# Kernel tuning notes

Hardware: AMD Instinct MI355X
Metric: run time of the kernel (lower is better)

Reference implementation:

```python
import jax, jax.numpy as jnp
import numpy as np

ND, NT = 30000, 15000
FD, FT = 200, 570
H = 768
E_DD, E_DT, E_TT = 300000, 400000, 200000
NEG_SLOPE = 0.2


def _gat(x_src, x_dst, src, dst, Ws, Wd, a_s, a_d, b, n_dst):
    # PyG GATConv, heads=1: hs = lin_src(x_src), hd = lin_dst(x_dst)
    hs = x_src @ Ws                       # [Ns, H]
    hd = x_dst @ Wd                       # [Nd, H]
    es = hs @ a_s                         # [Ns]
    ed = hd @ a_d                         # [Nd]
    e = jax.nn.leaky_relu(es[src] + ed[dst], negative_slope=NEG_SLOPE)  # [E]
    m = jax.ops.segment_max(e, dst, num_segments=n_dst)
    m = jnp.where(jnp.isfinite(m), m, 0.0)
    w = jnp.exp(e - m[dst])
    s = jax.ops.segment_sum(w, dst, num_segments=n_dst)
    alpha = w / (s[dst] + 1e-16)
    out = jax.ops.segment_sum(hs[src] * alpha[:, None], dst, num_segments=n_dst)  # [n_dst, H]
    return out + b


def _layer(xd, xt, dd_src, dd_dst, dt_src, dt_dst, tt_src, tt_dst, p):
    nd, nt = xd.shape[0], xt.shape[0]
    sl_d = jnp.arange(nd, dtype=dd_src.dtype)
    sl_t = jnp.arange(nt, dtype=tt_src.dtype)
    # add_self_loops=True for the homogeneous relations d-d and t-t
    dds = jnp.concatenate([dd_src, sl_d]); ddd = jnp.concatenate([dd_dst, sl_d])
    tts = jnp.concatenate([tt_src, sl_t]); ttd = jnp.concatenate([tt_dst, sl_t])
    o_dd = _gat(xd, xd, dds, ddd, p['Wsrc_dd'], p['Wdst_dd'], p['asrc_dd'], p['adst_dd'], p['b_dd'], nd)
    o_rv = _gat(xt, xd, dt_dst, dt_src, p['Wsrc_rv'], p['Wdst_rv'], p['asrc_rv'], p['adst_rv'], p['b_rv'], nd)
    o_dt = _gat(xd, xt, dt_src, dt_dst, p['Wsrc_dt'], p['Wdst_dt'], p['asrc_dt'], p['adst_dt'], p['b_dt'], nt)
    o_tt = _gat(xt, xt, tts, ttd, p['Wsrc_tt'], p['Wdst_tt'], p['asrc_tt'], p['adst_tt'], p['b_tt'], nt)
    # HeteroConv aggr='sum', then relu per node type
    return jax.nn.relu(o_dd + o_rv), jax.nn.relu(o_dt + o_tt)


def setup_inputs() -> dict:
    key = jax.random.key(0)
    ks = jax.random.split(key, 40)
    d = {}
    d['drug_x'] = jax.random.normal(ks[0], (ND, FD), jnp.float32)
    d['target_x'] = jax.random.normal(ks[1], (NT, FT), jnp.float32)
    d['dd_src'] = jax.random.randint(ks[2], (E_DD,), 0, ND, jnp.int32)
    d['dd_dst'] = jax.random.randint(ks[3], (E_DD,), 0, ND, jnp.int32)
    d['dt_src'] = jax.random.randint(ks[4], (E_DT,), 0, ND, jnp.int32)
    d['dt_dst'] = jax.random.randint(ks[5], (E_DT,), 0, NT, jnp.int32)
    d['tt_src'] = jax.random.randint(ks[6], (E_TT,), 0, NT, jnp.int32)
    d['tt_dst'] = jax.random.randint(ks[7], (E_TT,), 0, NT, jnp.int32)
    d['drug_mask'] = jax.random.randint(ks[8], (ND, 1), 0, 2, jnp.int32)
    d['target_mask'] = jax.random.randint(ks[9], (NT, 1), 0, 2, jnp.int32)
    d['mask_drug'] = 0.05 * jax.random.normal(ks[10], (1, FD), jnp.float32)
    d['mask_target'] = 0.05 * jax.random.normal(ks[11], (1, FT), jnp.float32)
    i = 12
    for rel, fin_s, fin_d in [('dd', FD, FD), ('dt', FD, FT), ('rv', FT, FD), ('tt', FT, FT)]:
        d['Wsrc_' + rel] = 0.05 * jax.random.normal(ks[i], (fin_s, H), jnp.float32); i += 1
        d['Wdst_' + rel] = 0.05 * jax.random.normal(ks[i], (fin_d, H), jnp.float32); i += 1
        d['asrc_' + rel] = 0.05 * jax.random.normal(ks[i], (H,), jnp.float32); i += 1
        d['adst_' + rel] = 0.05 * jax.random.normal(ks[i], (H,), jnp.float32); i += 1
        d['b_' + rel] = jnp.zeros((H,), jnp.float32)
    return d


def reference(drug_x, target_x, dd_src, dd_dst, dt_src, dt_dst, tt_src, tt_dst,
              drug_mask, target_mask, mask_drug, mask_target,
              Wsrc_dd, Wdst_dd, asrc_dd, adst_dd, b_dd,
              Wsrc_dt, Wdst_dt, asrc_dt, adst_dt, b_dt,
              Wsrc_rv, Wdst_rv, asrc_rv, adst_rv, b_rv,
              Wsrc_tt, Wdst_tt, asrc_tt, adst_tt, b_tt):
    p = dict(Wsrc_dd=Wsrc_dd, Wdst_dd=Wdst_dd, asrc_dd=asrc_dd, adst_dd=adst_dd, b_dd=b_dd,
             Wsrc_dt=Wsrc_dt, Wdst_dt=Wdst_dt, asrc_dt=asrc_dt, adst_dt=adst_dt, b_dt=b_dt,
             Wsrc_rv=Wsrc_rv, Wdst_rv=Wdst_rv, asrc_rv=asrc_rv, adst_rv=adst_rv, b_rv=b_rv,
             Wsrc_tt=Wsrc_tt, Wdst_tt=Wdst_tt, asrc_tt=asrc_tt, adst_tt=adst_tt, b_tt=b_tt)
    xd, xt = _layer(drug_x, target_x, dd_src, dd_dst, dt_src, dt_dst, tt_src, tt_dst, p)
    # MAE branch: replace masked node features with learned mask token, rerun conv
    dm = drug_mask.astype(jnp.float32)
    tm = target_mask.astype(jnp.float32)
    _dx = drug_x * (1.0 - dm) + dm * mask_drug
    _tx = target_x * (1.0 - tm) + tm * mask_target
    _xd, _xt = _layer(_dx, _tx, dd_src, dd_dst, dt_src, dt_dst, tt_src, tt_dst, p)
    loss_mae = (((xd - _xd) ** 2) * dm).sum() / (dm.sum() * H + 1e-16) \
             + (((xt - _xt) ** 2) * tm).sum() / (tm.sum() * H + 1e-16)
    return (xd, xt, loss_mae)
```

## Files before the change

### kernel.cpp

```cpp
#include <hip/hip_runtime.h>
#include <hip/hip_bf16.h>

#define ND 30000
#define NT 15000
#define FD 200
#define FT 570
#define HDIM 768
#define EDD 300000
#define EDT 400000
#define ETT 200000

#define KPD 256
#define KPT 576
#define KPA 832

#define BM 128
#define BN 128
#define GBK 64
#define MTD ((ND + BM - 1) / BM)
#define MTT ((NT + BM - 1) / BM)

typedef __attribute__((ext_vector_type(8))) short short8;
typedef __attribute__((ext_vector_type(4))) float float4v;


__device__ __forceinline__ float ldx(const void* p, size_t i, int f32) {
  return f32 ? ((const float*)p)[i]
             : __bfloat162float(((const __hip_bfloat16*)p)[i]);
}
__device__ __forceinline__ void stx(void* p, size_t i, int f32, float v) {
  if (f32) ((float*)p)[i] = v;
  else     ((__hip_bfloat16*)p)[i] = __float2bfloat16(v);
}
__device__ __forceinline__ float b2f(unsigned short u) {
  return __uint_as_float(((unsigned)u) << 16);
}
__device__ __forceinline__ unsigned short f2b(float f) {
  __hip_bfloat16 h = __float2bfloat16(f);
  return *(unsigned short*)&h;
}
__device__ __forceinline__ unsigned pk2(float a, float b) {
  return (unsigned)f2b(a) | ((unsigned)f2b(b) << 16);
}

__device__ __forceinline__ float wave_reduce(float v) {
#pragma unroll
  for (int off = 32; off > 0; off >>= 1) v += __shfl_xor(v, off, 64);
  return v;
}

__global__ void sniff(const void* x, int* flag) {
  int t = threadIdx.x;
  float cnt = 0.f;
  for (int i = t; i < 8192; i += 256) {
    float v = __bfloat162float(((const __hip_bfloat16*)x)[i]);
    if (!(fabsf(v) < 100.f)) cnt += 1.f;
  }
  cnt = wave_reduce(cnt);
  __shared__ float red[4];
  if ((t & 63) == 0) red[t >> 6] = cnt;
  __syncthreads();
  if (t == 0) flag[0] = (red[0] + red[1] + red[2] + red[3] > 256.f) ? 1 : 0;
}

__global__ __launch_bounds__(256) void wa_dot8(
    const void* W0, const void* W1, const void* W2, const void* W3,
    const void* W4, const void* W5, const void* W6, const void* W7,
    const void* a0, const void* a1, const void* a2, const void* a3,
    const void* a4, const void* a5, const void* a6, const void* a7,
    float* __restrict__ vaD, float* __restrict__ vaT,
    const int* __restrict__ flag) {
  const void* Ws[8] = {W0, W1, W2, W3, W4, W5, W6, W7};
  const void* as[8] = {a0, a1, a2, a3, a4, a5, a6, a7};
  int f32 = flag[0];
  int wid = (blockIdx.x * 256 + threadIdx.x) >> 6;
  int lane = threadIdx.x & 63;
  const void* W; const void* a; float* out; int k;
  if (wid < 4 * FD) {
    int q = wid / FD; k = wid - q * FD;
    W = Ws[q]; a = as[q]; out = vaD + q * FD + k;
  } else {
    int w2 = wid - 4 * FD;
    if (w2 >= 4 * FT) return;
    int q = w2 / FT; k = w2 - q * FT;
    W = Ws[4 + q]; a = as[4 + q]; out = vaT + q * FT + k;
  }
  float acc = 0.f;
  for (int h = lane; h < HDIM; h += 64)
    acc += ldx(W, (size_t)k * HDIM + h, f32) * ldx(a, h, f32);
  acc = wave_reduce(acc);
  if (lane == 0) *out = acc;
}

__global__ void tok_dots(const void* __restrict__ tok1, const void* __restrict__ tok2,
                         const float* __restrict__ vaD, const float* __restrict__ vaT,
                         float* __restrict__ ts, const int* __restrict__ flag) {
  int w = threadIdx.x >> 6;
  int lane = threadIdx.x & 63;
  int f32 = flag[0];
  float acc = 0.f;
  if (w < 4) {
    for (int k = lane; k < FD; k += 64) acc += ldx(tok1, k, f32) * vaD[w * FD + k];
  } else {
    int q = w - 4;
    for (int k = lane; k < FT; k += 64) acc += ldx(tok2, k, f32) * vaT[q * FT + k];
  }
  acc = wave_reduce(acc);
  if (lane == 0) {
    const int map[8] = {0, 1, 3, 4, 2, 5, 6, 7};
    ts[map[w]] = acc;
  }
}

__global__ __launch_bounds__(256) void row_dot4(const void* __restrict__ x,
                                                const float* __restrict__ va,
                                                float* __restrict__ outv, int N, int K,
                                                const int* __restrict__ flag) {
  int f32 = flag[0];
  int row = (blockIdx.x * 256 + threadIdx.x) >> 6;
  int lane = threadIdx.x & 63;
  if (row >= N) return;
  float a0 = 0.f, a1 = 0.f, a2 = 0.f, a3 = 0.f;
  for (int k = lane; k < K; k += 64) {
    float v = ldx(x, (size_t)row * K + k, f32);
    a0 += v * va[k];
    a1 += v * va[K + k];
    a2 += v * va[2 * K + k];
    a3 += v * va[3 * K + k];
  }
  a0 = wave_reduce(a0); a1 = wave_reduce(a1);
  a2 = wave_reduce(a2); a3 = wave_reduce(a3);
  if (lane == 0) {
    float* o = outv + (size_t)row * 4;
    o[0] = a0; o[1] = a1; o[2] = a2; o[3] = a3;
  }
}

__global__ __launch_bounds__(256) void pack_a(const void* __restrict__ x,
                                              unsigned short* __restrict__ Aout,
                                              int M, int K, int Kp,
                                              const int* __restrict__ flag) {
  int f32 = flag[0];
  long long gid = (long long)blockIdx.x * 256 + threadIdx.x;
  long long total = (long long)M * Kp / 4;
  if (gid >= total) return;
  long long e0 = gid * 4;
  int row = (int)(e0 / Kp);
  int k = (int)(e0 % Kp);
  ushort4 o;
  unsigned short r[4];
#pragma unroll
  for (int c = 0; c < 4; ++c) {
    int kk = k + c;
    float f = 0.f;
    if (kk < K) f = ldx(x, (size_t)row * K + kk, f32);
    r[c] = f2b(f);
  }
  o.x = r[0]; o.y = r[1]; o.z = r[2]; o.w = r[3];
  *(ushort4*)(Aout + e0) = o;
}

__global__ __launch_bounds__(256) void pack_bTa(const void* __restrict__ W1,
                                                const void* __restrict__ W2,
                                                unsigned short* __restrict__ Bout,
                                                const int* __restrict__ flag) {
  int f32 = flag[0];
  long long gid = (long long)blockIdx.x * 256 + threadIdx.x;
  long long total = (long long)HDIM * KPA / 4;
  if (gid >= total) return;
  long long e0 = gid * 4;
  int n = (int)(e0 / KPA);
  int k = (int)(e0 % KPA);
  ushort4 o;
  unsigned short r[4];
#pragma unroll
  for (int c = 0; c < 4; ++c) {
    int kk = k + c;
    float f = 0.f;
    if (kk < 256) {
      if (kk < FD) f = ldx(W1, (size_t)kk * HDIM + n, f32);
    } else {
      int k2 = kk - 256;
      if (k2 < FT) f = ldx(W2, (size_t)k2 * HDIM + n, f32);
    }
    r[c] = f2b(f);
  }
  o.x = r[0]; o.y = r[1]; o.z = r[2]; o.w = r[3];
  *(ushort4*)(Bout + e0) = o;
}

__global__ void zero_i32(int* __restrict__ p, int n) {
  int i = blockIdx.x * 256 + threadIdx.x;
  if (i < n) p[i] = 0;
}

__global__ void count4(const int* __restrict__ dd_dst, const int* __restrict__ dt_src,
                       const int* __restrict__ dt_dst, const int* __restrict__ tt_dst,
                       int* __restrict__ c_dd, int* __restrict__ c_rv,
                       int* __restrict__ c_dt, int* __restrict__ c_tt) {
  int i = blockIdx.x * 256 + threadIdx.x;
  if (i < EDD + ND) { int d = (i < EDD) ? dd_dst[i] : i - EDD; atomicAdd(&c_dd[d], 1); return; }
  i -= EDD + ND;
  if (i < EDT) { atomicAdd(&c_rv[dt_src[i]], 1); return; }
  i -= EDT;
  if (i < EDT) { atomicAdd(&c_dt[dt_dst[i]], 1); return; }
  i -= EDT;
  if (i < ETT + NT) { int d = (i < ETT) ? tt_dst[i] : i - ETT; atomicAdd(&c_tt[d], 1); }
}

__global__ __launch_bounds__(256) void scan6(
    const int* __restrict__ a0, int n0, int* __restrict__ o0,
    const int* __restrict__ a1, int n1, int* __restrict__ o1,
    const int* __restrict__ a2, int n2, int* __restrict__ o2,
    const int* __restrict__ a3, int n3, int* __restrict__ o3,
    const int* __restrict__ a4, int n4, int* __restrict__ o4,
    const int* __restrict__ a5, int n5, int* __restrict__ o5) {
  const int* a; int n; int* o;
  switch (blockIdx.x) {
    case 0: a = a0; n = n0; o = o0; break;
    case 1: a = a1; n = n1; o = o1; break;
    case 2: a = a2; n = n2; o = o2; break;
    case 3: a = a3; n = n3; o = o3; break;
    case 4: a = a4; n = n4; o = o4; break;
    default: a = a5; n = n5; o = o5; break;
  }
  __shared__ int part[256];
  int t = threadIdx.x;
  int strip = (n + 255) / 256;
  int lo = min(t * strip, n), hi = min(lo + strip, n);
  int s = 0;
  for (int i = lo; i < hi; ++i) s += a[i];
  part[t] = s;
  __syncthreads();
  if (t == 0) {
    int run = 0;
    for (int i = 0; i < 256; ++i) { int v = part[i]; part[i] = run; run += v; }
  }
  __syncthreads();
  int run = part[t];
  for (int i = lo; i < hi; ++i) { o[i] = run; run += a[i]; }
  if (hi == n) o[n] = run;
}

__global__ void ridx2(const int* __restrict__ mD, const int* __restrict__ cD,
                      int* __restrict__ rD,
                      const int* __restrict__ mT, const int* __restrict__ cT,
                      int* __restrict__ rT) {
  int i = blockIdx.x * 256 + threadIdx.x;
  if (i < ND) { if (mD[i] != 0) rD[cD[i]] = i; return; }
  i -= ND;
  if (i < NT) { if (mT[i] != 0) rT[cT[i]] = i; }
}

__global__ void fill4(const int* __restrict__ dd_src, const int* __restrict__ dd_dst,
                      const int* __restrict__ dt_src, const int* __restrict__ dt_dst,
                      const int* __restrict__ tt_src, const int* __restrict__ tt_dst,
                      const int* __restrict__ rp_dd, int* __restrict__ f_dd, int* __restrict__ ei_dd,
                      const int* __restrict__ rp_rv, int* __restrict__ f_rv, int* __restrict__ ei_rv,
                      const int* __restrict__ rp_dt, int* __restrict__ f_dt, int* __restrict__ ei_dt,
                      const int* __restrict__ rp_tt, int* __restrict__ f_tt, int* __restrict__ ei_tt) {
  int i = blockIdx.x * 256 + threadIdx.x;
  if (i < EDD + ND) {
    int s, d;
    if (i < EDD) { s = dd_src[i]; d = dd_dst[i]; } else { s = d = i - EDD; }
    ei_dd[rp_dd[d] + atomicAdd(&f_dd[d], 1)] = s;
    return;
  }
  i -= EDD + ND;
  if (i < EDT) {
    int d = dt_src[i], s = dt_dst[i];
    ei_rv[rp_rv[d] + atomicAdd(&f_rv[d], 1)] = s;
    return;
  }
  i -= EDT;
  if (i < EDT) {
    int d = dt_dst[i], s = dt_src[i];
    ei_dt[rp_dt[d] + atomicAdd(&f_dt[d], 1)] = s;
    return;
  }
  i -= EDT;
  if (i < ETT + NT) {
    int s, d;
    if (i < ETT) { s = tt_src[i]; d = tt_dst[i]; } else { s = d = i - ETT; }
    ei_tt[rp_tt[d] + atomicAdd(&f_tt[d], 1)] = s;
  }
}


__device__ __forceinline__ void fma4(float* acc, uint2 A, float al) {
  unsigned w;
  w = A.x; acc[0] += al * __uint_as_float(w << 16); acc[1] += al * __uint_as_float(w & 0xffff0000u);
  w = A.y; acc[2] += al * __uint_as_float(w << 16); acc[3] += al * __uint_as_float(w & 0xffff0000u);
}

__device__ __forceinline__ float lrexp(float v) {
  v = (v >= 0.f) ? v : 0.2f * v;
  return __expf(v);
}

__global__ __launch_bounds__(256) void gat_agg2(
    const int* __restrict__ rp1, const int* __restrict__ ei1,
    const unsigned short* __restrict__ A1, const int* __restrict__ msk1,
    const void* __restrict__ tok1,
    const float* __restrict__ es1, const float* __restrict__ ed1,
    const int* __restrict__ rp2, const int* __restrict__ ei2,
    const unsigned short* __restrict__ A2, const int* __restrict__ msk2,
    const void* __restrict__ tok2,
    const float* __restrict__ es2, const float* __restrict__ ed2,
    const float* __restrict__ ts,
    int N, const int* __restrict__ mdst, const int* __restrict__ cidx,
    unsigned short* __restrict__ agg1, unsigned short* __restrict__ agg2,
    const int* __restrict__ flag) {
  int wid = (blockIdx.x * 256 + threadIdx.x) >> 6;
  int lane = threadIdx.x & 63;
  if (wid >= N) return;
  int f32 = flag[0];
  bool need2 = (mdst[wid] != 0);
  float ac1[13], ac2[13];
#pragma unroll
  for (int c = 0; c < 13; ++c) { ac1[c] = 0.f; ac2[c] = 0.f; }

  {
    float tes = ts[0], ted = ts[1];
    int lo = rp1[wid], hi = rp1[wid + 1];
    float edA = ed1[4 * (size_t)wid];
    float s1 = 0.f, s2 = 0.f;
    for (int e = lo + lane; e < hi; e += 64) {
      int sn = ei1[e];
      float ev = es1[4 * (size_t)sn];
      s1 += lrexp(ev + edA);
      if (need2) {
        float e2 = (msk1[sn] != 0) ? tes : ev;
        s2 += lrexp(e2 + ted);
      }
    }
    s1 = wave_reduce(s1);
    float i1 = 1.f / (s1 + 1e-16f), i2 = 0.f;
    if (need2) { s2 = wave_reduce(s2); i2 = 1.f / (s2 + 1e-16f); }
    float wt = 0.f;
    int pn = (lo < hi) ? ei1[lo] : 0;
    for (int e = lo; e < hi; ++e) {
      int sn = __builtin_amdgcn_readfirstlane(pn);
      if (e + 1 < hi) pn = ei1[e + 1];
      uint2 rv = *(const uint2*)(A1 + (size_t)sn * KPD + 4 * lane);
      float ev = es1[4 * (size_t)sn];
      fma4(ac1, rv, lrexp(ev + edA) * i1);
      if (need2) {
        if (msk1[sn] != 0) wt += lrexp(tes + ted) * i2;
        else fma4(ac2, rv, lrexp(ev + ted) * i2);
      }
    }
    if (need2) {
#pragma unroll
      for (int c = 0; c < 4; ++c) {
        int col = 4 * lane + c;
        float tv = (col < FD) ? ldx(tok1, col, f32) : 0.f;
        ac2[c] += wt * tv;
      }
    }
  }

  {
    float tes = ts[2], ted = ts[3];
    int lo = rp2[wid], hi = rp2[wid + 1];
    float edA = ed2[4 * (size_t)wid];
    float s1 = 0.f, s2 = 0.f;
    for (int e = lo + lane; e < hi; e += 64) {
      int sn = ei2[e];
      float ev = es2[4 * (size_t)sn];
      s1 += lrexp(ev + edA);
      if (need2) {
        float e2 = (msk2[sn] != 0) ? tes : ev;
        s2 += lrexp(e2 + ted);
      }
    }
    s1 = wave_reduce(s1);
    float i1 = 1.f / (s1 + 1e-16f), i2 = 0.f;
    if (need2) { s2 = wave_reduce(s2); i2 = 1.f / (s2 + 1e-16f); }
    float wt = 0.f;
    int pn = (lo < hi) ? ei2[lo] : 0;
    for (int e = lo; e < hi; ++e) {
      int sn = __builtin_amdgcn_readfirstlane(pn);
      if (e + 1 < hi) pn = ei2[e + 1];
      const unsigned short* row = A2 + (size_t)sn * KPT;
      uint2 ra = *(const uint2*)(row + 4 * lane);
      uint2 rb = *(const uint2*)(row + 256 + 4 * lane);
      unsigned short rc = row[512 + lane];
      float ev = es2[4 * (size_t)sn];
      float a1 = lrexp(ev + edA) * i1;
      fma4(ac1 + 4, ra, a1);
      fma4(ac1 + 8, rb, a1);
      ac1[12] += a1 * b2f(rc);
      if (need2) {
        if (msk2[sn] != 0) {
          wt += lrexp(tes + ted) * i2;
        } else {
          float a2 = lrexp(ev + ted) * i2;
          fma4(ac2 + 4, ra, a2);
          fma4(ac2 + 8, rb, a2);
          ac2[12] += a2 * b2f(rc);
        }
      }
    }
    if (need2) {
#pragma unroll
      for (int c = 0; c < 4; ++c) {
        int colA = 4 * lane + c;
        int colB = 256 + 4 * lane + c;
        ac2[4 + c] += wt * ldx(tok2, colA, f32);
        ac2[8 + c] += wt * ldx(tok2, colB, f32);
      }
      int colC = 512 + lane;
      ac2[12] += wt * ((colC < FT) ? ldx(tok2, colC, f32) : 0.f);
    }
  }

  unsigned short* o1 = agg1 + (size_t)wid * KPA;
  uint2 u;
  u.x = pk2(ac1[0], ac1[1]);  u.y = pk2(ac1[2], ac1[3]);  *(uint2*)(o1 + 4 * lane) = u;
  u.x = pk2(ac1[4], ac1[5]);  u.y = pk2(ac1[6], ac1[7]);  *(uint2*)(o1 + 256 + 4 * lane) = u;
  u.x = pk2(ac1[8], ac1[9]);  u.y = pk2(ac1[10], ac1[11]); *(uint2*)(o1 + 512 + 4 * lane) = u;
  o1[768 + lane] = f2b(ac1[12]);
  if (need2) {
    unsigned short* o2 = agg2 + (size_t)cidx[wid] * KPA;
    u.x = pk2(ac2[0], ac2[1]);  u.y = pk2(ac2[2], ac2[3]);  *(uint2*)(o2 + 4 * lane) = u;
    u.x = pk2(ac2[4], ac2[5]);  u.y = pk2(ac2[6], ac2[7]);  *(uint2*)(o2 + 256 + 4 * lane) = u;
    u.x = pk2(ac2[8], ac2[9]);  u.y = pk2(ac2[10], ac2[11]); *(uint2*)(o2 + 512 + 4 * lane) = u;
    o2[768 + lane] = f2b(ac2[12]);
  }
}


__global__ __launch_bounds__(256) void gemm2(
    const unsigned short* __restrict__ A0, const unsigned short* __restrict__ B0,
    const void* __restrict__ c1_0, const void* __restrict__ c2_0,
    int M0s, const int* __restrict__ mc0, const int* __restrict__ rx0,
    unsigned long long base0, float* __restrict__ pp0,
    const unsigned short* __restrict__ A1, const unsigned short* __restrict__ B1,
    const void* __restrict__ c1_1, const void* __restrict__ c2_1,
    int M1s, const int* __restrict__ mc1, const int* __restrict__ rx1,
    unsigned long long base1, float* __restrict__ pp1,
    int mt0, int nwg, void* __restrict__ out, int mode,
    const int* __restrict__ flag) {
  __shared__ unsigned long long lds8[8192];
  unsigned short* ldsS = (unsigned short*)lds8;
  float* Cls = (float*)lds8;

  int b = blockIdx.x;
  int q = nwg >> 3, r = nwg & 7;
  int xcd = b & 7, pos = b >> 3;
  int wg = (xcd < r ? xcd * (q + 1) : r * (q + 1) + (xcd - r) * q) + pos;
  int prob = (wg >= 6 * mt0) ? 1 : 0;
  int rel = prob ? (wg - 6 * mt0) : wg;
  int mt = rel / 6, nt = rel - mt * 6;

  const unsigned short* A = prob ? A1 : A0;
  const unsigned short* Bt = prob ? B1 : B0;
  const void* c1 = prob ? c1_1 : c1_0;
  const void* c2 = prob ? c2_1 : c2_0;
  const int* mc = prob ? mc1 : mc0;
  const int* ridx = prob ? rx1 : rx0;
  size_t base = prob ? base1 : base0;
  float* parts = prob ? pp1 : pp0;
  int M = prob ? M1s : M0s;
  if (mc) M = *mc;
  int m0 = mt * BM;
  if (m0 >= M) return;
  int n0 = nt * BN;

  int t = threadIdx.x;
  int wave = t >> 6, lane = t & 63;
  int quad = lane >> 4, l15 = lane & 15;
  int wrow = (wave & 1) * 64, wcol = (wave >> 1) * 64;
  float4v acc[4][4];
#pragma unroll
  for (int i = 0; i < 4; ++i)
#pragma unroll
    for (int j = 0; j < 4; ++j) acc[i][j] = (float4v){0.f, 0.f, 0.f, 0.f};

  auto stage = [&](int buf, int k0) {
#pragma unroll
    for (int i = 0; i < 4; ++i) {
      int chunk = (wave * 4 + i) * 64 + lane;
      int row = chunk >> 3;
      int cs = (chunk & 7) ^ (row & 7);
      const unsigned short* ga = A + (size_t)(m0 + row) * KPA + k0 + cs * 8;
      __builtin_amdgcn_global_load_lds(
          (const __attribute__((address_space(1))) unsigned int*)ga,
          (__attribute__((address_space(3))) unsigned int*)(ldsS + buf * 8192 + (wave * 4 + i) * 512),
          16, 0, 0);
      const unsigned short* gb = Bt + (size_t)(n0 + row) * KPA + k0 + cs * 8;
      __builtin_amdgcn_global_load_lds(
          (const __attribute__((address_space(1))) unsigned int*)gb,
          (__attribute__((address_space(3))) unsigned int*)(ldsS + 16384 + buf * 8192 + (wave * 4 + i) * 512),
          16, 0, 0);
    }
  };
  auto compute = [&](int buf) {
#pragma unroll
    for (int kk = 0; kk < 2; ++kk) {
      int kc = kk * 4 + quad;
      short8 a[4], bfr[4];
#pragma unroll
      for (int i = 0; i < 4; ++i) {
        int rr = wrow + i * 16 + l15;
        a[i] = *(const short8*)(ldsS + buf * 8192 + rr * 64 + ((kc ^ (rr & 7)) << 3));
      }
#pragma unroll
      for (int j = 0; j < 4; ++j) {
        int rr = wcol + j * 16 + l15;
        bfr[j] = *(const short8*)(ldsS + 16384 + buf * 8192 + rr * 64 + ((kc ^ (rr & 7)) << 3));
      }
#pragma unroll
      for (int i = 0; i < 4; ++i)
#pragma unroll
        for (int j = 0; j < 4; ++j)
          acc[i][j] = __builtin_amdgcn_mfma_f32_16x16x32_bf16(a[i], bfr[j], acc[i][j], 0, 0, 0);
    }
  };

  stage(0, 0);
  __syncthreads();
  int cur = 0;
#pragma unroll 1
  for (int ks = 1; ks < KPA / GBK; ++ks) {
    stage(cur ^ 1, ks * GBK);
    compute(cur);
    __syncthreads();
    cur ^= 1;
  }
  compute(cur);

  int f32 = flag[0];
  float bias[4];
#pragma unroll
  for (int j = 0; j < 4; ++j) {
    int n = n0 + wcol + j * 16 + l15;
    bias[j] = ldx(c1, n, f32) + ldx(c2, n, f32);
  }
  __syncthreads();
#pragma unroll
  for (int i = 0; i < 4; ++i) {
#pragma unroll
    for (int j = 0; j < 4; ++j) {
      int col = wcol + j * 16 + l15;
#pragma unroll
      for (int rr = 0; rr < 4; ++rr) {
        int row = wrow + i * 16 + quad * 4 + rr;
        float v = acc[i][j][rr] + bias[j];
        Cls[row * 128 + col] = v > 0.f ? v : 0.f;
      }
    }
  }
  __syncthreads();
  float cpart = 0.f;
#pragma unroll
  for (int i = 0; i < 16; ++i) {
    int ch = t + i * 256;
    int row = ch >> 5, cc = ch & 31;
    int m = m0 + row;
    if (m >= M) continue;
    float v0 = Cls[row * 128 + cc * 4 + 0];
    float v1 = Cls[row * 128 + cc * 4 + 1];
    float v2 = Cls[row * 128 + cc * 4 + 2];
    float v3 = Cls[row * 128 + cc * 4 + 3];
    int n = n0 + cc * 4;
    if (mode == 1) {
      size_t idx = base + (size_t)m * HDIM + n;
      if (f32) {
        *(float4v*)((float*)out + idx) = (float4v){v0, v1, v2, v3};
      } else {
        uint2 u; u.x = pk2(v0, v1); u.y = pk2(v2, v3);
        *(uint2*)((unsigned short*)out + idx) = u;
      }
    } else {
      int orig = ridx[m];
      size_t idx = base + (size_t)orig * HDIM + n;
      float d0, d1, d2, d3;
      if (f32) {
        float4v w = *(const float4v*)((const float*)out + idx);
        d0 = w[0] - v0; d1 = w[1] - v1; d2 = w[2] - v2; d3 = w[3] - v3;
      } else {
        uint2 u = *(const uint2*)((const unsigned short*)out + idx);
        d0 = __uint_as_float(u.x << 16) - v0;
        d1 = __uint_as_float(u.x & 0xffff0000u) - v1;
        d2 = __uint_as_float(u.y << 16) - v2;
        d3 = __uint_as_float(u.y & 0xffff0000u) - v3;
      }
      cpart += d0 * d0 + d1 * d1 + d2 * d2 + d3 * d3;
    }
  }
  if (mode == 2) {
    cpart = wave_reduce(cpart);
    if (lane == 0) atomicAdd(&parts[(wg * 4 + wave) & 2047], cpart);
  }
}

__global__ __launch_bounds__(256) void loss_final(const float* __restrict__ parts,
                                                  const int* __restrict__ cd,
                                                  const int* __restrict__ ct,
                                                  void* __restrict__ out, size_t off,
                                                  const int* __restrict__ flag) {
  float a = 0.f, b = 0.f;
  for (int i = threadIdx.x; i < 2048; i += 256) { a += parts[i]; b += parts[2048 + i]; }
  a = wave_reduce(a);
  b = wave_reduce(b);
  __shared__ float ra[4], rb[4];
  if ((threadIdx.x & 63) == 0) { ra[threadIdx.x >> 6] = a; rb[threadIdx.x >> 6] = b; }
  __syncthreads();
  if (threadIdx.x == 0) {
    float sd = ra[0] + ra[1] + ra[2] + ra[3];
    float st = rb[0] + rb[1] + rb[2] + rb[3];
    float loss = sd / ((float)cd[0] * (float)HDIM + 1e-16f)
               + st / ((float)ct[0] * (float)HDIM + 1e-16f);
    stx(out, off, flag[0], loss);
  }
}


extern "C" void kernel_launch(void* const* d_in, const int* in_sizes, int n_in,
                              void* d_out, int out_size, void* d_ws, size_t ws_size,
                              hipStream_t stream) {
  const void* drug_x    = d_in[0];
  const void* target_x  = d_in[1];
  const int* dd_src = (const int*)d_in[2];
  const int* dd_dst = (const int*)d_in[3];
  const int* dt_src = (const int*)d_in[4];
  const int* dt_dst = (const int*)d_in[5];
  const int* tt_src = (const int*)d_in[6];
  const int* tt_dst = (const int*)d_in[7];
  const int* drug_mask   = (const int*)d_in[8];
  const int* target_mask = (const int*)d_in[9];
  const void* mask_drug   = d_in[10];
  const void* mask_target = d_in[11];
  const void* Wsrc_dd = d_in[12]; const void* Wdst_dd = d_in[13];
  const void* asrc_dd = d_in[14]; const void* adst_dd = d_in[15];
  const void* b_dd    = d_in[16];
  const void* Wsrc_dt = d_in[17]; const void* Wdst_dt = d_in[18];
  const void* asrc_dt = d_in[19]; const void* adst_dt = d_in[20];
  const void* b_dt    = d_in[21];
  const void* Wsrc_rv = d_in[22]; const void* Wdst_rv = d_in[23];
  const void* asrc_rv = d_in[24]; const void* adst_rv = d_in[25];
  const void* b_rv    = d_in[26];
  const void* Wsrc_tt = d_in[27]; const void* Wdst_tt = d_in[28];
  const void* asrc_tt = d_in[29]; const void* adst_tt = d_in[30];
  const void* b_tt    = d_in[31];

  char* p = (char*)d_ws;
  auto alloc = [&](size_t bytes) -> void* {
    void* r = (void*)p;
    p += (bytes + 255) & ~(size_t)255;
    return r;
  };
  const size_t PAD = (size_t)BM * KPA * 2;
  unsigned short* Ad    = (unsigned short*)alloc((size_t)ND * KPD * 2);
  unsigned short* At    = (unsigned short*)alloc((size_t)NT * KPT * 2);
  unsigned short* aggd1 = (unsigned short*)alloc((size_t)ND * KPA * 2 + PAD);
  unsigned short* aggd2 = (unsigned short*)alloc((size_t)ND * KPA * 2 + PAD);
  unsigned short* aggt1 = (unsigned short*)alloc((size_t)NT * KPA * 2 + PAD);
  unsigned short* aggt2 = (unsigned short*)alloc((size_t)NT * KPA * 2 + PAD);
  unsigned short* BdW   = (unsigned short*)alloc((size_t)HDIM * KPA * 2);
  unsigned short* BtW   = (unsigned short*)alloc((size_t)HDIM * KPA * 2);
  float* dvec1 = (float*)alloc((size_t)ND * 4 * 4);
  float* tvec1 = (float*)alloc((size_t)NT * 4 * 4);
  int* rp_dd = (int*)alloc((size_t)(ND + 1) * 4);
  int* rp_rv = (int*)alloc((size_t)(ND + 1) * 4);
  int* rp_dt = (int*)alloc((size_t)(NT + 1) * 4);
  int* rp_tt = (int*)alloc((size_t)(NT + 1) * 4);
  int* ei_dd = (int*)alloc((size_t)(EDD + ND) * 4);
  int* ei_rv = (int*)alloc((size_t)EDT * 4);
  int* ei_dt = (int*)alloc((size_t)EDT * 4);
  int* ei_tt = (int*)alloc((size_t)(ETT + NT) * 4);
  const int ZN = 4 * (ND + NT) + 4096;
  int* zblock = (int*)alloc((size_t)ZN * 4);
  int* cnt_dd = zblock;
  int* cnt_rv = cnt_dd + ND;
  int* cnt_dt = cnt_rv + ND;
  int* cnt_tt = cnt_dt + NT;
  int* f_dd   = cnt_tt + NT;
  int* f_rv   = f_dd + ND;
  int* f_dt   = f_rv + ND;
  int* f_tt   = f_dt + NT;
  float* parts = (float*)(f_tt + NT);
  int* cidxD = (int*)alloc((size_t)(ND + 1) * 4);
  int* cidxT = (int*)alloc((size_t)(NT + 1) * 4);
  int* ridxD = (int*)alloc((size_t)ND * 4);
  int* ridxT = (int*)alloc((size_t)NT * 4);
  float* vaD = (float*)alloc((size_t)4 * FD * 4);
  float* vaT = (float*)alloc((size_t)4 * FT * 4);
  float* tokscal = (float*)alloc(64);
  int*   flag  = (int*)alloc(256);

  sniff<<<1, 256, 0, stream>>>(drug_x, flag);
  zero_i32<<<(ZN + 255) / 256, 256, 0, stream>>>(zblock, ZN);

  {
    int waves = 4 * FD + 4 * FT;
    wa_dot8<<<(waves * 64 + 255) / 256, 256, 0, stream>>>(
        Wsrc_dd, Wdst_dd, Wdst_rv, Wsrc_dt, Wsrc_rv, Wdst_dt, Wsrc_tt, Wdst_tt,
        asrc_dd, adst_dd, adst_rv, asrc_dt, asrc_rv, adst_dt, asrc_tt, adst_tt,
        vaD, vaT, flag);
    tok_dots<<<1, 512, 0, stream>>>(mask_drug, mask_target, vaD, vaT, tokscal, flag);
  }

  {
    int g = (int)(((long long)HDIM * KPA / 4 + 255) / 256);
    pack_bTa<<<g, 256, 0, stream>>>(Wsrc_dd, Wsrc_rv, BdW, flag);
    pack_bTa<<<g, 256, 0, stream>>>(Wsrc_dt, Wsrc_tt, BtW, flag);
  }

  {
    int total = (EDD + ND) + EDT + EDT + (ETT + NT);
    count4<<<(total + 255) / 256, 256, 0, stream>>>(dd_dst, dt_src, dt_dst, tt_dst,
                                                    cnt_dd, cnt_rv, cnt_dt, cnt_tt);
    scan6<<<6, 256, 0, stream>>>(cnt_dd, ND, rp_dd, cnt_rv, ND, rp_rv,
                                 cnt_dt, NT, rp_dt, cnt_tt, NT, rp_tt,
                                 drug_mask, ND, cidxD, target_mask, NT, cidxT);
    ridx2<<<(ND + NT + 255) / 256, 256, 0, stream>>>(drug_mask, cidxD, ridxD,
                                                     target_mask, cidxT, ridxT);
    fill4<<<(total + 255) / 256, 256, 0, stream>>>(dd_src, dd_dst, dt_src, dt_dst,
                                                   tt_src, tt_dst,
                                                   rp_dd, f_dd, ei_dd, rp_rv, f_rv, ei_rv,
                                                   rp_dt, f_dt, ei_dt, rp_tt, f_tt, ei_tt);
  }

  {
    long long ta = (long long)ND * KPD / 4;
    pack_a<<<(int)((ta + 255) / 256), 256, 0, stream>>>(drug_x, Ad, ND, FD, KPD, flag);
    ta = (long long)NT * KPT / 4;
    pack_a<<<(int)((ta + 255) / 256), 256, 0, stream>>>(target_x, At, NT, FT, KPT, flag);
  }
  row_dot4<<<(ND + 3) / 4, 256, 0, stream>>>(drug_x, vaD, dvec1, ND, FD, flag);
  row_dot4<<<(NT + 3) / 4, 256, 0, stream>>>(target_x, vaT, tvec1, NT, FT, flag);

  gat_agg2<<<(ND + 3) / 4, 256, 0, stream>>>(
      rp_dd, ei_dd, Ad, drug_mask, mask_drug, dvec1 + 0, dvec1 + 1,
      rp_rv, ei_rv, At, target_mask, mask_target, tvec1 + 0, dvec1 + 2,
      tokscal, ND, drug_mask, cidxD, aggd1, aggd2, flag);
  gat_agg2<<<(NT + 3) / 4, 256, 0, stream>>>(
      rp_dt, ei_dt, Ad, drug_mask, mask_drug, dvec1 + 3, tvec1 + 1,
      rp_tt, ei_tt, At, target_mask, mask_target, tvec1 + 2, tvec1 + 3,
      tokscal + 4, NT, target_mask, cidxT, aggt1, aggt2, flag);

  size_t baseT = (size_t)ND * HDIM;
  size_t baseL = baseT + (size_t)NT * HDIM;

  const int NWG = 6 * (MTD + MTT);
  gemm2<<<NWG, 256, 0, stream>>>(
      aggd1, BdW, b_dd, b_rv, ND, nullptr, nullptr, 0ULL, parts,
      aggt1, BtW, b_dt, b_tt, NT, nullptr, nullptr, (unsigned long long)baseT, parts,
      MTD, NWG, d_out, 1, flag);
  gemm2<<<NWG, 256, 0, stream>>>(
      aggd2, BdW, b_dd, b_rv, ND, cidxD + ND, ridxD, 0ULL, parts,
      aggt2, BtW, b_dt, b_tt, NT, cidxT + NT, ridxT, (unsigned long long)baseT, parts + 2048,
      MTD, NWG, d_out, 2, flag);

  loss_final<<<1, 256, 0, stream>>>(parts, cidxD + ND, cidxT + NT, d_out, baseL, flag);
}
```

Baseline: 923.5 us.

## Fuse pack/rowdot and agg launches, halve GEMM K-tile and LDS footprint

Merges the bf16 packing of the node features with the per-row attention dot products into one kernel, so each input row is read once. It also merges the two pack_bTa launches and the two gat_agg2 launches into single launches. The GEMM K-tile drops from 64 to 32 with a matching swizzle, which halves shared memory, and the epilogue now writes C through LDS in two 64-column halves. The aim is fewer launches, less input traffic and higher GEMM occupancy, at the cost of more K iterations and barriers in the GEMM.

```diff
diff --git a/kernel.cpp b/kernel.cpp
--- a/kernel.cpp
+++ b/kernel.cpp
@@ -16,7 +16,8 @@
 
 #define BM 128
 #define BN 128
-#define GBK 64
+#define GBK 32
+#define KTILES (KPA / GBK)
 #define MTD ((ND + BM - 1) / BM)
 #define MTT ((NT + BM - 1) / BM)
 
@@ -112,21 +113,45 @@
   }
 }
 
-__global__ __launch_bounds__(256) void row_dot4(const void* __restrict__ x,
-                                                const float* __restrict__ va,
-                                                float* __restrict__ outv, int N, int K,
-                                                const int* __restrict__ flag) {
+__global__ __launch_bounds__(256) void pack_rowdot(
+    const void* __restrict__ xD, const void* __restrict__ xT,
+    const float* __restrict__ vaD, const float* __restrict__ vaT,
+    unsigned short* __restrict__ Ad, unsigned short* __restrict__ At,
+    float* __restrict__ dvec, float* __restrict__ tvec,
+    const int* __restrict__ flag) {
+  int wid = (blockIdx.x * 256 + threadIdx.x) >> 6;
+  int lane = threadIdx.x & 63;
   int f32 = flag[0];
-  int row = (blockIdx.x * 256 + threadIdx.x) >> 6;
-  int lane = threadIdx.x & 63;
-  if (row >= N) return;
+  const void* x; const float* va; unsigned short* Aout; float* outv; int K, Kp, row;
+  if (wid < ND) { x = xD; va = vaD; Aout = Ad; outv = dvec; K = FD; Kp = KPD; row = wid; }
+  else if (wid < ND + NT) { x = xT; va = vaT; Aout = At; outv = tvec; K = FT; Kp = KPT; row = wid - ND; }
+  else return;
   float a0 = 0.f, a1 = 0.f, a2 = 0.f, a3 = 0.f;
-  for (int k = lane; k < K; k += 64) {
-    float v = ldx(x, (size_t)row * K + k, f32);
-    a0 += v * va[k];
-    a1 += v * va[K + k];
-    a2 += v * va[2 * K + k];
-    a3 += v * va[3 * K + k];
+  for (int it = 0; it * 256 < Kp; ++it) {
+    int base = 4 * lane + it * 256;
+    if (base >= Kp) continue;
+    ushort4 o;
+    unsigned short r[4];
+    float fv[4];
+#pragma unroll
+    for (int c = 0; c < 4; ++c) {
+      int kk = base + c;
+      float f = (kk < K) ? ldx(x, (size_t)row * K + kk, f32) : 0.f;
+      fv[c] = f;
+      r[c] = f2b(f);
+    }
+    o.x = r[0]; o.y = r[1]; o.z = r[2]; o.w = r[3];
+    *(ushort4*)(Aout + (size_t)row * Kp + base) = o;
+#pragma unroll
+    for (int c = 0; c < 4; ++c) {
+      int kk = base + c;
+      if (kk < K) {
+        a0 += fv[c] * va[kk];
+        a1 += fv[c] * va[K + kk];
+        a2 += fv[c] * va[2 * K + kk];
+        a3 += fv[c] * va[3 * K + kk];
+      }
+    }
   }
   a0 = wave_reduce(a0); a1 = wave_reduce(a1);
   a2 = wave_reduce(a2); a3 = wave_reduce(a3);
@@ -136,38 +161,17 @@
   }
 }
 
-__global__ __launch_bounds__(256) void pack_a(const void* __restrict__ x,
-                                              unsigned short* __restrict__ Aout,
-                                              int M, int K, int Kp,
-                                              const int* __restrict__ flag) {
+__global__ __launch_bounds__(256) void pack_bTa2(
+    const void* __restrict__ W1a, const void* __restrict__ W2a, unsigned short* __restrict__ Ba,
+    const void* __restrict__ W1b, const void* __restrict__ W2b, unsigned short* __restrict__ Bb,
+    const int* __restrict__ flag) {
   int f32 = flag[0];
+  long long one = (long long)HDIM * KPA / 4;
   long long gid = (long long)blockIdx.x * 256 + threadIdx.x;
-  long long total = (long long)M * Kp / 4;
-  if (gid >= total) return;
-  long long e0 = gid * 4;
-  int row = (int)(e0 / Kp);
-  int k = (int)(e0 % Kp);
-  ushort4 o;
-  unsigned short r[4];
-#pragma unroll
-  for (int c = 0; c < 4; ++c) {
-    int kk = k + c;
-    float f = 0.f;
-    if (kk < K) f = ldx(x, (size_t)row * K + kk, f32);
-    r[c] = f2b(f);
-  }
-  o.x = r[0]; o.y = r[1]; o.z = r[2]; o.w = r[3];
-  *(ushort4*)(Aout + e0) = o;
-}
-
-__global__ __launch_bounds__(256) void pack_bTa(const void* __restrict__ W1,
-                                                const void* __restrict__ W2,
-                                                unsigned short* __restrict__ Bout,
-                                                const int* __restrict__ flag) {
-  int f32 = flag[0];
-  long long gid = (long long)blockIdx.x * 256 + threadIdx.x;
-  long long total = (long long)HDIM * KPA / 4;
-  if (gid >= total) return;
+  if (gid >= 2 * one) return;
+  const void* W1; const void* W2; unsigned short* Bout;
+  if (gid < one) { W1 = W1a; W2 = W2a; Bout = Ba; }
+  else { W1 = W1b; W2 = W2b; Bout = Bb; gid -= one; }
   long long e0 = gid * 4;
   int n = (int)(e0 / KPA);
   int k = (int)(e0 % KPA);
@@ -286,7 +290,6 @@
   }
 }
 
-
 __device__ __forceinline__ void fma4(float* acc, uint2 A, float al) {
   unsigned w;
   w = A.x; acc[0] += al * __uint_as_float(w << 16); acc[1] += al * __uint_as_float(w & 0xffff0000u);
@@ -299,22 +302,45 @@
 }
 
 __global__ __launch_bounds__(256) void gat_agg2(
-    const int* __restrict__ rp1, const int* __restrict__ ei1,
-    const unsigned short* __restrict__ A1, const int* __restrict__ msk1,
-    const void* __restrict__ tok1,
-    const float* __restrict__ es1, const float* __restrict__ ed1,
-    const int* __restrict__ rp2, const int* __restrict__ ei2,
-    const unsigned short* __restrict__ A2, const int* __restrict__ msk2,
-    const void* __restrict__ tok2,
-    const float* __restrict__ es2, const float* __restrict__ ed2,
-    const float* __restrict__ ts,
-    int N, const int* __restrict__ mdst, const int* __restrict__ cidx,
-    unsigned short* __restrict__ agg1, unsigned short* __restrict__ agg2,
+    const unsigned short* __restrict__ A1, const unsigned short* __restrict__ A2,
+    const int* __restrict__ msk1, const int* __restrict__ msk2,
+    const void* __restrict__ tok1, const void* __restrict__ tok2,
+    const float* __restrict__ tokscal,
+    const int* __restrict__ rpD1, const int* __restrict__ eiD1,
+    const float* __restrict__ esD1, const float* __restrict__ edD1,
+    const int* __restrict__ rpD2, const int* __restrict__ eiD2,
+    const float* __restrict__ esD2, const float* __restrict__ edD2,
+    const int* __restrict__ cidxD,
+    unsigned short* __restrict__ aggd1, unsigned short* __restrict__ aggd2,
+    const int* __restrict__ rpT1, const int* __restrict__ eiT1,
+    const float* __restrict__ esT1, const float* __restrict__ edT1,
+    const int* __restrict__ rpT2, const int* __restrict__ eiT2,
+    const float* __restrict__ esT2, const float* __restrict__ edT2,
+    const int* __restrict__ cidxT,
+    unsigned short* __restrict__ aggt1, unsigned short* __restrict__ aggt2,
     const int* __restrict__ flag) {
-  int wid = (blockIdx.x * 256 + threadIdx.x) >> 6;
+  int gwid = (blockIdx.x * 256 + threadIdx.x) >> 6;
   int lane = threadIdx.x & 63;
-  if (wid >= N) return;
+  if (gwid >= ND + NT) return;
   int f32 = flag[0];
+
+  const int *rp1, *ei1, *rp2, *ei2, *cidx;
+  const float *es1, *ed1, *es2, *ed2, *ts;
+  const int* mdst;
+  unsigned short *agg1, *agg2;
+  int wid;
+  if (gwid < ND) {
+    wid = gwid; mdst = msk1;
+    rp1 = rpD1; ei1 = eiD1; es1 = esD1; ed1 = edD1;
+    rp2 = rpD2; ei2 = eiD2; es2 = esD2; ed2 = edD2;
+    cidx = cidxD; agg1 = aggd1; agg2 = aggd2; ts = tokscal;
+  } else {
+    wid = gwid - ND; mdst = msk2;
+    rp1 = rpT1; ei1 = eiT1; es1 = esT1; ed1 = edT1;
+    rp2 = rpT2; ei2 = eiT2; es2 = esT2; ed2 = edT2;
+    cidx = cidxT; agg1 = aggt1; agg2 = aggt2; ts = tokscal + 4;
+  }
+
   bool need2 = (mdst[wid] != 0);
   float ac1[13], ac2[13];
 #pragma unroll
@@ -442,7 +468,7 @@
     unsigned long long base1, float* __restrict__ pp1,
     int mt0, int nwg, void* __restrict__ out, int mode,
     const int* __restrict__ flag) {
-  __shared__ unsigned long long lds8[8192];
+  __shared__ unsigned long long lds8[4096];
   unsigned short* ldsS = (unsigned short*)lds8;
   float* Cls = (float*)lds8;
 
@@ -480,50 +506,46 @@
 
   auto stage = [&](int buf, int k0) {
 #pragma unroll
-    for (int i = 0; i < 4; ++i) {
-      int chunk = (wave * 4 + i) * 64 + lane;
-      int row = chunk >> 3;
-      int cs = (chunk & 7) ^ (row & 7);
+    for (int i = 0; i < 2; ++i) {
+      int chunk = (wave * 2 + i) * 64 + lane;
+      int row = chunk >> 2;
+      int cs = (chunk & 3) ^ ((row >> 1) & 3);
       const unsigned short* ga = A + (size_t)(m0 + row) * KPA + k0 + cs * 8;
       __builtin_amdgcn_global_load_lds(
           (const __attribute__((address_space(1))) unsigned int*)ga,
-          (__attribute__((address_space(3))) unsigned int*)(ldsS + buf * 8192 + (wave * 4 + i) * 512),
+          (__attribute__((address_space(3))) unsigned int*)(ldsS + buf * 4096 + (wave * 2 + i) * 512),
           16, 0, 0);
       const unsigned short* gb = Bt + (size_t)(n0 + row) * KPA + k0 + cs * 8;
       __builtin_amdgcn_global_load_lds(
           (const __attribute__((address_space(1))) unsigned int*)gb,
-          (__attribute__((address_space(3))) unsigned int*)(ldsS + 16384 + buf * 8192 + (wave * 4 + i) * 512),
+          (__attribute__((address_space(3))) unsigned int*)(ldsS + 8192 + buf * 4096 + (wave * 2 + i) * 512),
           16, 0, 0);
     }
   };
   auto compute = [&](int buf) {
-#pragma unroll
-    for (int kk = 0; kk < 2; ++kk) {
-      int kc = kk * 4 + quad;
-      short8 a[4], bfr[4];
-#pragma unroll
-      for (int i = 0; i < 4; ++i) {
-        int rr = wrow + i * 16 + l15;
-        a[i] = *(const short8*)(ldsS + buf * 8192 + rr * 64 + ((kc ^ (rr & 7)) << 3));
-      }
-#pragma unroll
-      for (int j = 0; j < 4; ++j) {
-        int rr = wcol + j * 16 + l15;
-        bfr[j] = *(const short8*)(ldsS + 16384 + buf * 8192 + rr * 64 + ((kc ^ (rr & 7)) << 3));
-      }
-#pragma unroll
-      for (int i = 0; i < 4; ++i)
-#pragma unroll
-        for (int j = 0; j < 4; ++j)
-          acc[i][j] = __builtin_amdgcn_mfma_f32_16x16x32_bf16(a[i], bfr[j], acc[i][j], 0, 0, 0);
-    }
+    short8 a[4], bfr[4];
+#pragma unroll
+    for (int i = 0; i < 4; ++i) {
+      int rr = wrow + i * 16 + l15;
+      a[i] = *(const short8*)(ldsS + buf * 4096 + rr * 32 + ((quad ^ ((rr >> 1) & 3)) << 3));
+    }
+#pragma unroll
+    for (int j = 0; j < 4; ++j) {
+      int rc = wcol + j * 16 + l15;
+      bfr[j] = *(const short8*)(ldsS + 8192 + buf * 4096 + rc * 32 + ((quad ^ ((rc >> 1) & 3)) << 3));
+    }
+#pragma unroll
+    for (int i = 0; i < 4; ++i)
+#pragma unroll
+      for (int j = 0; j < 4; ++j)
+        acc[i][j] = __builtin_amdgcn_mfma_f32_16x16x32_bf16(a[i], bfr[j], acc[i][j], 0, 0, 0);
   };
 
   stage(0, 0);
   __syncthreads();
   int cur = 0;
 #pragma unroll 1
-  for (int ks = 1; ks < KPA / GBK; ++ks) {
+  for (int ks = 1; ks < KTILES; ++ks) {
     stage(cur ^ 1, ks * GBK);
     compute(cur);
     __syncthreads();
@@ -538,56 +560,57 @@
     int n = n0 + wcol + j * 16 + l15;
     bias[j] = ldx(c1, n, f32) + ldx(c2, n, f32);
   }
-  __syncthreads();
-#pragma unroll
-  for (int i = 0; i < 4; ++i) {
-#pragma unroll
-    for (int j = 0; j < 4; ++j) {
-      int col = wcol + j * 16 + l15;
-#pragma unroll
-      for (int rr = 0; rr < 4; ++rr) {
-        int row = wrow + i * 16 + quad * 4 + rr;
-        float v = acc[i][j][rr] + bias[j];
-        Cls[row * 128 + col] = v > 0.f ? v : 0.f;
+  float cpart = 0.f;
+#pragma unroll
+  for (int h = 0; h < 2; ++h) {
+    __syncthreads();
+    if ((wave >> 1) == h) {
+#pragma unroll
+      for (int i = 0; i < 4; ++i)
+#pragma unroll
+        for (int j = 0; j < 4; ++j)
+#pragma unroll
+          for (int rr = 0; rr < 4; ++rr) {
+            int row = wrow + i * 16 + quad * 4 + rr;
+            int col = (j * 16 + l15) ^ (((row >> 2) & 1) << 4);
+            float v = acc[i][j][rr] + bias[j];
+            Cls[row * 64 + col] = v > 0.f ? v : 0.f;
+          }
+    }
+    __syncthreads();
+#pragma unroll
+    for (int i = 0; i < 8; ++i) {
+      int ch = t + i * 256;
+      int row = ch >> 4, cc = ch & 15;
+      int m = m0 + row;
+      if (m >= M) continue;
+      int scc = cc ^ (((row >> 2) & 1) << 2);
+      float4v v = *(const float4v*)(Cls + row * 64 + scc * 4);
+      int n = n0 + h * 64 + cc * 4;
+      if (mode == 1) {
+        size_t idx = base + (size_t)m * HDIM + n;
+        if (f32) {
+          *(float4v*)((float*)out + idx) = v;
+        } else {
+          uint2 u; u.x = pk2(v[0], v[1]); u.y = pk2(v[2], v[3]);
+          *(uint2*)((unsigned short*)out + idx) = u;
+        }
+      } else {
+        int orig = ridx[m];
+        size_t idx = base + (size_t)orig * HDIM + n;
+        float d0, d1, d2, d3;
+        if (f32) {
+          float4v w = *(const float4v*)((const float*)out + idx);
+          d0 = w[0] - v[0]; d1 = w[1] - v[1]; d2 = w[2] - v[2]; d3 = w[3] - v[3];
+        } else {
+          uint2 u = *(const uint2*)((const unsigned short*)out + idx);
+          d0 = __uint_as_float(u.x << 16) - v[0];
+          d1 = __uint_as_float(u.x & 0xffff0000u) - v[1];
+          d2 = __uint_as_float(u.y << 16) - v[2];
+          d3 = __uint_as_float(u.y & 0xffff0000u) - v[3];
+        }
+        cpart += d0 * d0 + d1 * d1 + d2 * d2 + d3 * d3;
       }
-    }
-  }
-  __syncthreads();
-  float cpart = 0.f;
-#pragma unroll
-  for (int i = 0; i < 16; ++i) {
-    int ch = t + i * 256;
-    int row = ch >> 5, cc = ch & 31;
-    int m = m0 + row;
-    if (m >= M) continue;
-    float v0 = Cls[row * 128 + cc * 4 + 0];
-    float v1 = Cls[row * 128 + cc * 4 + 1];
-    float v2 = Cls[row * 128 + cc * 4 + 2];
-    float v3 = Cls[row * 128 + cc * 4 + 3];
-    int n = n0 + cc * 4;
-    if (mode == 1) {
-      size_t idx = base + (size_t)m * HDIM + n;
-      if (f32) {
-        *(float4v*)((float*)out + idx) = (float4v){v0, v1, v2, v3};
-      } else {
-        uint2 u; u.x = pk2(v0, v1); u.y = pk2(v2, v3);
-        *(uint2*)((unsigned short*)out + idx) = u;
-      }
-    } else {
-      int orig = ridx[m];
-      size_t idx = base + (size_t)orig * HDIM + n;
-      float d0, d1, d2, d3;
-      if (f32) {
-        float4v w = *(const float4v*)((const float*)out + idx);
-        d0 = w[0] - v0; d1 = w[1] - v1; d2 = w[2] - v2; d3 = w[3] - v3;
-      } else {
-        uint2 u = *(const uint2*)((const unsigned short*)out + idx);
-        d0 = __uint_as_float(u.x << 16) - v0;
-        d1 = __uint_as_float(u.x & 0xffff0000u) - v1;
-        d2 = __uint_as_float(u.y << 16) - v2;
-        d3 = __uint_as_float(u.y & 0xffff0000u) - v3;
-      }
-      cpart += d0 * d0 + d1 * d1 + d2 * d2 + d3 * d3;
     }
   }
   if (mode == 2) {
@@ -704,9 +727,9 @@
   }
 
   {
-    int g = (int)(((long long)HDIM * KPA / 4 + 255) / 256);
-    pack_bTa<<<g, 256, 0, stream>>>(Wsrc_dd, Wsrc_rv, BdW, flag);
-    pack_bTa<<<g, 256, 0, stream>>>(Wsrc_dt, Wsrc_tt, BtW, flag);
+    long long tb = 2 * ((long long)HDIM * KPA / 4);
+    pack_bTa2<<<(int)((tb + 255) / 256), 256, 0, stream>>>(Wsrc_dd, Wsrc_rv, BdW,
+                                                           Wsrc_dt, Wsrc_tt, BtW, flag);
   }
 
   {
@@ -724,23 +747,17 @@
                                                    rp_dt, f_dt, ei_dt, rp_tt, f_tt, ei_tt);
   }
 
-  {
-    long long ta = (long long)ND * KPD / 4;
-    pack_a<<<(int)((ta + 255) / 256), 256, 0, stream>>>(drug_x, Ad, ND, FD, KPD, flag);
-    ta = (long long)NT * KPT / 4;
-    pack_a<<<(int)((ta + 255) / 256), 256, 0, stream>>>(target_x, At, NT, FT, KPT, flag);
-  }
-  row_dot4<<<(ND + 3) / 4, 256, 0, stream>>>(drug_x, vaD, dvec1, ND, FD, flag);
-  row_dot4<<<(NT + 3) / 4, 256, 0, stream>>>(target_x, vaT, tvec1, NT, FT, flag);
-
-  gat_agg2<<<(ND + 3) / 4, 256, 0, stream>>>(
-      rp_dd, ei_dd, Ad, drug_mask, mask_drug, dvec1 + 0, dvec1 + 1,
-      rp_rv, ei_rv, At, target_mask, mask_target, tvec1 + 0, dvec1 + 2,
-      tokscal, ND, drug_mask, cidxD, aggd1, aggd2, flag);
-  gat_agg2<<<(NT + 3) / 4, 256, 0, stream>>>(
-      rp_dt, ei_dt, Ad, drug_mask, mask_drug, dvec1 + 3, tvec1 + 1,
-      rp_tt, ei_tt, At, target_mask, mask_target, tvec1 + 2, tvec1 + 3,
-      tokscal + 4, NT, target_mask, cidxT, aggt1, aggt2, flag);
+  pack_rowdot<<<((ND + NT) * 64 + 255) / 256, 256, 0, stream>>>(
+      drug_x, target_x, vaD, vaT, Ad, At, dvec1, tvec1, flag);
+
+  gat_agg2<<<(ND + NT + 3) / 4, 256, 0, stream>>>(
+      Ad, At, drug_mask, target_mask, mask_drug, mask_target, tokscal,
+      rp_dd, ei_dd, dvec1 + 0, dvec1 + 1,
+      rp_rv, ei_rv, tvec1 + 0, dvec1 + 2,
+      cidxD, aggd1, aggd2,
+      rp_dt, ei_dt, dvec1 + 3, tvec1 + 1,
+      rp_tt, ei_tt, tvec1 + 2, tvec1 + 3,
+      cidxT, aggt1, aggt2, flag);
 
   size_t baseT = (size_t)ND * HDIM;
   size_t baseL = baseT + (size_t)NT * HDIM;
```

New measurement: 945.4 us. 2.4% more time.
